# Performance work log

Hardware: AMD Instinct MI355X
Metric: run time of the kernel (lower is better)

Reference implementation:

```python
import jax, jax.numpy as jnp
import numpy as np

FSIZE = 128   # fsize
ANUM = 16     # number of agents
CNUM = 2048   # number of cities
BATCH = 64


def setup_inputs() -> dict:
    key = jax.random.key(0)
    ks = jax.random.split(key, 6)
    f = FSIZE
    N = CNUM + 2 * ANUM
    s = 0.02
    return {
        "nfeature": jax.random.normal(ks[0], (BATCH, f, N), jnp.float32),
        # torch Linear weights are [out, in]
        "Wg": jax.random.normal(ks[1], (f, 4 * f), jnp.float32) * s,   # glb_embedding
        "bg": jnp.zeros((f,), jnp.float32),
        "Wc": jax.random.normal(ks[2], (3 * f, 2 * f), jnp.float32) * s,  # city_embedding
        "bc": jnp.zeros((3 * f,), jnp.float32),
        "Wa": jax.random.normal(ks[3], (f, 3 * f), jnp.float32) * s,   # agent_embedding
        "ba": jnp.zeros((f,), jnp.float32),
        "Wp": jax.random.normal(ks[4], (f, f), jnp.float32) * s,       # project_out
        "bp": jnp.zeros((f,), jnp.float32),
        "step": 1,
        "anum": ANUM,
    }


def reference(nfeature, Wg, bg, Wc, bc, Wa, ba, Wp, bp, step, anum):
    nf = jnp.transpose(nfeature, (0, 2, 1))  # [B, N, f]
    B, N, f = nf.shape
    cnum = N - 2 * anum
    city = nf[:, :cnum]                       # [B, cnum, f]
    a_start = nf[:, cnum:cnum + anum]         # [B, anum, f]
    a_end = nf[:, cnum + anum:]               # [B, anum, f]

    # global context via max pooling over segments -> glb_embedding
    glb = jnp.concatenate([nf.max(1), city.max(1), a_start.max(1), a_end.max(1)], axis=1)  # [B, 4f]
    deglb = (glb @ Wg.T + bg)[:, None, :]     # [B, 1, f]

    # mean-pooled global context -> same glb_embedding -> free agent token
    ave = jnp.concatenate([nf.mean(1), city.mean(1), a_start.mean(1), a_end.mean(1)], axis=1)
    free_agent = (ave @ Wg.T + bg)[:, None, :]  # [B, 1, f]

    # city keys/values/logit-keys: x, y, z
    city_feat = jnp.concatenate([jnp.broadcast_to(deglb, (B, cnum, f)), city], axis=2)  # [B, cnum, 2f]
    xyz = city_feat @ Wc.T + bc               # [B, cnum, 3f]
    x, y, z = jnp.split(xyz, 3, axis=2)       # each [B, cnum, f]

    # agent queries
    agent_feat = jnp.concatenate(
        [jnp.broadcast_to(deglb, (B, anum, f)), a_start, a_end], axis=2)  # [B, anum, 3f]
    af = agent_feat @ Wa.T + ba               # [B, anum, f]
    if step > 0:
        af = jnp.concatenate([af, free_agent], axis=1)  # [B, anum+1, f]

    scale = 1.0 / jnp.sqrt(jnp.float32(f))
    ucj = jnp.einsum('baf,bcf->bac', af, x) * scale           # [B, A, cnum]
    new_af = jnp.einsum('bac,bcf->baf', jax.nn.softmax(ucj, axis=2), y)
    new_af = new_af @ Wp.T + bp                                # project_out
    logits = jnp.tanh(jnp.einsum('baf,bcf->bac', new_af, z) * scale) * 10.0  # [B, A, cnum]
    probs = jax.nn.softmax(jnp.transpose(logits, (0, 2, 1)), axis=2)         # [B, cnum, A]
    return probs
```

## Files before the change

kernel.cpp:

```cpp
#include <hip/hip_runtime.h>
#include <math.h>

#define F 128
#define NTOT 2080
#define CN 2048
#define AN 16
#define NA 17
#define CHK 128
#define NCHK 16

__device__ __forceinline__ float wmax(float v){
  #pragma unroll
  for(int m=32;m;m>>=1) v = fmaxf(v, __shfl_xor(v, m, 64));
  return v;
}
__device__ __forceinline__ float wsum(float v){
  #pragma unroll
  for(int m=32;m;m>>=1) v += __shfl_xor(v, m, 64);
  return v;
}

__global__ __launch_bounds__(256) void k0t_transpose(
      const float* __restrict__ Wg, const float* __restrict__ Wc,
      const float* __restrict__ Wp, const float* __restrict__ Wa,
      float* __restrict__ WgT, float* __restrict__ WcT,
      float* __restrict__ WpT, float* __restrict__ WaT){
  __shared__ float tile[32][33];
  const int z = blockIdx.z;
  const float* src; float* dst; int R, C;
  if(z==0){ src=Wg; dst=WgT; R=128; C=512; }
  else if(z==1){ src=Wc; dst=WcT; R=384; C=256; }
  else if(z==2){ src=Wp; dst=WpT; R=128; C=128; }
  else { src=Wa; dst=WaT; R=128; C=384; }
  const int c0 = blockIdx.x*32, r0 = blockIdx.y*32;
  if(c0>=C || r0>=R) return;
  const int tx = threadIdx.x&31, ty = threadIdx.x>>5;
  #pragma unroll
  for(int rr=0;rr<4;rr++)
    tile[ty+rr*8][tx] = src[(size_t)(r0+ty+rr*8)*C + c0 + tx];
  __syncthreads();
  #pragma unroll
  for(int rr=0;rr<4;rr++)
    dst[(size_t)(c0+ty+rr*8)*R + r0 + tx] = tile[tx][ty+rr*8];
}

__global__ __launch_bounds__(128) void k0a_wpy(const float* __restrict__ Wp, const float* __restrict__ Wc,
                                               float* __restrict__ Wpy){
  const int k = blockIdx.x, i = threadIdx.x;
  float acc = 0.f;
  const float* wp = Wp + (size_t)k*F;
  for(int j=0;j<F;j++) acc += wp[j]*Wc[(size_t)(128+j)*256 + 128 + i];
  Wpy[k*F+i] = acc;
}

__global__ __launch_bounds__(128) void k0b_m1(const float* __restrict__ Wc, const float* __restrict__ Wpy,
                                              float* __restrict__ M1){
  const int jc = blockIdx.x, i = threadIdx.x;
  float acc = 0.f;
  for(int k=0;k<F;k++) acc += Wc[(size_t)(256+k)*256 + 128 + jc]*Wpy[k*F+i];
  M1[jc*F+i] = acc;
}

__global__ __launch_bounds__(256) void k1_reduce(const float* __restrict__ nf,
                                                 float* __restrict__ glb, float* __restrict__ ave){
  const int jg = blockIdx.x, b = blockIdx.y;
  const int w = threadIdx.x>>6, lane = threadIdx.x&63;
  const int j = jg*4 + w;
  const float4* row = (const float4*)(nf + (size_t)(b*F + j)*NTOT);
  float cmax=-INFINITY, csum=0.f, smax=-INFINITY, ssum=0.f, emax=-INFINITY, esum=0.f;
  for(int n4 = lane; n4 < 520; n4 += 64){
    float4 v = row[n4];
    float mx = fmaxf(fmaxf(v.x,v.y), fmaxf(v.z,v.w));
    float sm = (v.x+v.y)+(v.z+v.w);
    if(n4 < 512){ cmax=fmaxf(cmax,mx); csum+=sm; }
    else if(n4 < 516){ smax=fmaxf(smax,mx); ssum+=sm; }
    else { emax=fmaxf(emax,mx); esum+=sm; }
  }
  cmax=wmax(cmax); csum=wsum(csum); smax=wmax(smax); ssum=wsum(ssum); emax=wmax(emax); esum=wsum(esum);
  if(lane==0){
    const int gb = b*4*F;
    glb[gb + j]       = fmaxf(cmax, fmaxf(smax,emax));
    glb[gb + F + j]   = cmax;
    glb[gb + 2*F + j] = smax;
    glb[gb + 3*F + j] = emax;
    float tS = csum+ssum+esum;
    ave[gb + j]       = tS / 2080.f;
    ave[gb + F + j]   = csum / 2048.f;
    ave[gb + 2*F + j] = ssum / 16.f;
    ave[gb + 3*F + j] = esum / 16.f;
  }
}

__global__ __launch_bounds__(256) void k2a_prep(
    const float* __restrict__ WgT, const float* __restrict__ bg,
    const float* __restrict__ WcT, const float* __restrict__ Wc, const float* __restrict__ bc,
    const float* __restrict__ WpT, const float* __restrict__ bp,
    const float* __restrict__ Wpy,
    const float* __restrict__ glb, const float* __restrict__ ave,
    float* __restrict__ deglb_g, float* __restrict__ fa_g, float* __restrict__ cx,
    float* __restrict__ czc, float* __restrict__ vz, float* __restrict__ szc){
  const int b = blockIdx.x, tid = threadIdx.x;
  __shared__ float glb_s[512], ave_s[512];
  __shared__ float deglb_s[F], cvec_s[3*F], cpy_s[F];
  for(int i=tid;i<512;i+=256){ glb_s[i]=glb[b*512+i]; ave_s[i]=ave[b*512+i]; }
  __syncthreads();
  {
    const int j = tid&127;
    const float* src = (tid<128)? glb_s : ave_s;
    float a0=0.f,a1=0.f,a2=0.f,a3=0.f;
    for(int k=0;k<512;k+=4){
      a0 += WgT[(size_t)(k+0)*128+j]*src[k+0];
      a1 += WgT[(size_t)(k+1)*128+j]*src[k+1];
      a2 += WgT[(size_t)(k+2)*128+j]*src[k+2];
      a3 += WgT[(size_t)(k+3)*128+j]*src[k+3];
    }
    float d = (a0+a1)+(a2+a3) + bg[j];
    if(tid<128){ deglb_s[j]=d; deglb_g[b*F+j]=d; }
    else fa_g[b*F+j]=d;
  }
  __syncthreads();
  for(int i=tid;i<3*F;i+=256){
    float a0=0.f,a1=0.f,a2=0.f,a3=0.f;
    for(int k=0;k<F;k+=4){
      a0 += WcT[(size_t)(k+0)*384+i]*deglb_s[k+0];
      a1 += WcT[(size_t)(k+1)*384+i]*deglb_s[k+1];
      a2 += WcT[(size_t)(k+2)*384+i]*deglb_s[k+2];
      a3 += WcT[(size_t)(k+3)*384+i]*deglb_s[k+3];
    }
    float v = (a0+a1)+(a2+a3) + bc[i];
    cvec_s[i]=v;
    if(i<F) cx[b*F+i]=v;
  }
  __syncthreads();
  if(tid<128){
    const int j = tid;
    float a0=0.f,a1=0.f,a2=0.f,a3=0.f;
    for(int k=0;k<F;k+=4){
      a0 += WpT[(size_t)(k+0)*128+j]*cvec_s[128+k+0];
      a1 += WpT[(size_t)(k+1)*128+j]*cvec_s[128+k+1];
      a2 += WpT[(size_t)(k+2)*128+j]*cvec_s[128+k+2];
      a3 += WpT[(size_t)(k+3)*128+j]*cvec_s[128+k+3];
    }
    cpy_s[j] = (a0+a1)+(a2+a3) + bp[j];
  } else {
    const int j = tid-128;
    float a0=0.f,a1=0.f,a2=0.f,a3=0.f;
    for(int k=0;k<F;k+=4){
      a0 += Wpy[(size_t)(k+0)*128+j]*cvec_s[256+k+0];
      a1 += Wpy[(size_t)(k+1)*128+j]*cvec_s[256+k+1];
      a2 += Wpy[(size_t)(k+2)*128+j]*cvec_s[256+k+2];
      a3 += Wpy[(size_t)(k+3)*128+j]*cvec_s[256+k+3];
    }
    vz[b*F+j] = (a0+a1)+(a2+a3);
  }
  __syncthreads();
  if(tid<128){
    const int j = tid;
    float a0=0.f,a1=0.f,a2=0.f,a3=0.f;
    for(int k=0;k<F;k+=4){
      a0 += Wc[(size_t)(256+k+0)*256 + 128 + j]*cpy_s[k+0];
      a1 += Wc[(size_t)(256+k+1)*256 + 128 + j]*cpy_s[k+1];
      a2 += Wc[(size_t)(256+k+2)*256 + 128 + j]*cpy_s[k+2];
      a3 += Wc[(size_t)(256+k+3)*256 + 128 + j]*cpy_s[k+3];
    }
    czc[b*F+j] = (a0+a1)+(a2+a3);
  } else if(tid<192){
    const int lane = tid-128;
    float p = cpy_s[lane]*cvec_s[256+lane] + cpy_s[64+lane]*cvec_s[256+64+lane];
    p = wsum(p);
    if(lane==0) szc[b]=p;
  }
}

__global__ __launch_bounds__(256) void k2c_agents(
    const float* __restrict__ nf, const float* __restrict__ WaT, const float* __restrict__ ba,
    const float* __restrict__ Wc,
    const float* __restrict__ deglb_g, const float* __restrict__ fa_g, const float* __restrict__ cx,
    float* __restrict__ afx, float* __restrict__ sx){
  const int a = blockIdx.x, b = blockIdx.y, tid = threadIdx.x;
  __shared__ float src_s[384];
  __shared__ float af_s[F], cx_s[F];
  if(tid<128){ src_s[tid] = deglb_g[b*F+tid]; cx_s[tid]=cx[b*F+tid]; }
  else if(a<16){
    const int j = tid-128;
    src_s[128+j] = nf[(size_t)(b*F+j)*NTOT + CN + a];
    src_s[256+j] = nf[(size_t)(b*F+j)*NTOT + CN + AN + a];
  }
  __syncthreads();
  if(a<16){
    if(tid<128){
      const int j = tid;
      float a0=0.f,a1=0.f,a2=0.f,a3=0.f;
      for(int k=0;k<384;k+=4){
        a0 += WaT[(size_t)(k+0)*128+j]*src_s[k+0];
        a1 += WaT[(size_t)(k+1)*128+j]*src_s[k+1];
        a2 += WaT[(size_t)(k+2)*128+j]*src_s[k+2];
        a3 += WaT[(size_t)(k+3)*128+j]*src_s[k+3];
      }
      af_s[j] = (a0+a1)+(a2+a3) + ba[j];
    }
  } else if(tid<128){
    af_s[tid] = fa_g[b*F+tid];
  }
  __syncthreads();
  if(tid<128){
    const int j = tid;
    float a0=0.f,a1=0.f,a2=0.f,a3=0.f;
    for(int i=0;i<F;i+=4){
      a0 += af_s[i+0]*Wc[(size_t)(i+0)*256 + 128 + j];
      a1 += af_s[i+1]*Wc[(size_t)(i+1)*256 + 128 + j];
      a2 += af_s[i+2]*Wc[(size_t)(i+2)*256 + 128 + j];
      a3 += af_s[i+3]*Wc[(size_t)(i+3)*256 + 128 + j];
    }
    afx[((size_t)b*NA+a)*F + j] = (a0+a1)+(a2+a3);
  } else if(tid<192){
    const int lane = tid-128;
    float p = af_s[lane]*cx_s[lane] + af_s[64+lane]*cx_s[64+lane];
    p = wsum(p);
    if(lane==0) sx[b*NA+a]=p;
  }
}

__global__ __launch_bounds__(256) void k35_flash(const float* __restrict__ nf,
      const float* __restrict__ afx, const float* __restrict__ sx,
      float* __restrict__ pmax, float* __restrict__ psum, float* __restrict__ tpart){
  const int b = blockIdx.y, tid = threadIdx.x;
  const int chunk = blockIdx.x, c0 = chunk*CHK;
  __shared__ float afx_s[NA*F];
  __shared__ float sx_s[NA];
  __shared__ float at_s[NA*CHK];
  __shared__ float4 nf4_s[F*8];
  __shared__ float red_s[2][NA];
  __shared__ float m_s[NA];
  for(int o=tid;o<NA*F;o+=256) afx_s[o]=afx[(size_t)b*NA*F+o];
  if(tid<NA) sx_s[tid]=sx[b*NA+tid];
  __syncthreads();
  const int h = tid>>7, cl = tid&127, i0 = h*64;
  float acc[NA];
  #pragma unroll
  for(int a=0;a<NA;a++) acc[a]=0.f;
  {
    const float* base = nf + (size_t)b*F*NTOT + (size_t)i0*NTOT + c0 + cl;
    for(int q=0;q<16;q++){
      float v0 = base[(size_t)(q*4+0)*NTOT];
      float v1 = base[(size_t)(q*4+1)*NTOT];
      float v2 = base[(size_t)(q*4+2)*NTOT];
      float v3 = base[(size_t)(q*4+3)*NTOT];
      #pragma unroll
      for(int a=0;a<NA;a++){
        float4 w = *(const float4*)&afx_s[a*F + i0 + q*4];
        acc[a] += w.x*v0 + w.y*v1 + w.z*v2 + w.w*v3;
      }
    }
  }
  if(h==0){
    #pragma unroll
    for(int a=0;a<NA;a++) at_s[a*CHK+cl] = acc[a];
  }
  __syncthreads();
  const int lane = tid&63;
  const float scale = 0.088388347648318447f;
  if(h==1){
    const int wq = (tid>>6)&1;
    #pragma unroll
    for(int a=0;a<NA;a++){
      acc[a] = (acc[a] + at_s[a*CHK+cl] + sx_s[a])*scale;
      float m = wmax(acc[a]);
      if(lane==0) red_s[wq][a]=m;
    }
  }
  __syncthreads();
  if(tid<NA){
    float m = fmaxf(red_s[0][tid], red_s[1][tid]);
    m_s[tid]=m;
    pmax[(b*NA+tid)*NCHK + chunk]=m;
  }
  __syncthreads();
  if(h==1){
    const int wq = (tid>>6)&1;
    #pragma unroll
    for(int a=0;a<NA;a++){
      float e = __expf(acc[a]-m_s[a]);
      at_s[a*CHK+cl]=e;
      float s = wsum(e);
      if(lane==0) red_s[wq][a]=s;
    }
  }
  __syncthreads();
  if(tid<NA)
    psum[(b*NA+tid)*NCHK + chunk] = red_s[0][tid]+red_s[1][tid];
  const int i = tid&127, A0 = h*8;
  float ta[9];
  #pragma unroll
  for(int a=0;a<9;a++) ta[a]=0.f;
  for(int s4=0;s4<4;s4++){
    const int csl = s4*32, cs = c0 + csl;
    __syncthreads();
    for(int idx=tid; idx<F*8; idx+=256){
      const int ii=idx>>3, g=idx&7;
      nf4_s[ii*8 + (g^(ii&7))] = *(const float4*)(nf + (size_t)(b*F+ii)*NTOT + cs + g*4);
    }
    __syncthreads();
    #pragma unroll 2
    for(int g=0; g<8; g++){
      float4 v = nf4_s[i*8 + (g^(i&7))];
      #pragma unroll
      for(int a=0;a<9;a++){
        float4 w = *(const float4*)&at_s[(A0+a)*CHK + csl + g*4];
        ta[a] += w.x*v.x + w.y*v.y + w.z*v.z + w.w*v.w;
      }
    }
  }
  float* dst = tpart + (size_t)chunk*64*NA*F + (size_t)b*NA*F;
  #pragma unroll
  for(int a=0;a<9;a++){
    if(h==0 || a>0) dst[(A0+a)*F + i] = ta[a];
  }
}

__global__ __launch_bounds__(128) void k5c_final(const float* __restrict__ M1,
      const float* __restrict__ tpart, const float* __restrict__ pmax, const float* __restrict__ psum,
      const float* __restrict__ czc, const float* __restrict__ vz, const float* __restrict__ szc,
      float* __restrict__ afz, float* __restrict__ szv){
  const int a = blockIdx.x, b = blockIdx.y, tid = threadIdx.x;
  __shared__ float tn_s[F];
  const float* pm = pmax + (b*NA+a)*NCHK;
  const float* ps = psum + (b*NA+a)*NCHK;
  float M=-INFINITY;
  #pragma unroll
  for(int k=0;k<NCHK;k++) M = fmaxf(M, pm[k]);
  float w[NCHK]; float rs=0.f;
  #pragma unroll
  for(int k=0;k<NCHK;k++){ w[k]=__expf(pm[k]-M); rs += ps[k]*w[k]; }
  float s = 0.f;
  #pragma unroll
  for(int k=0;k<NCHK;k++) s += tpart[(size_t)k*64*NA*F + ((size_t)b*NA+a)*F + tid]*w[k];
  tn_s[tid] = s / rs;
  __syncthreads();
  float acc = 0.f;
  const float* m = M1 + (size_t)tid*F;
  for(int i=0;i<F;i++) acc += m[i]*tn_s[i];
  afz[((size_t)b*NA+a)*F + tid] = acc + czc[b*F+tid];
  float p = tn_s[tid]*vz[b*F+tid];
  p = wsum(p);
  __shared__ float red[2];
  if((tid&63)==0) red[tid>>6]=p;
  __syncthreads();
  if(tid==0) szv[b*NA+a] = red[0]+red[1] + szc[b];
}

__global__ __launch_bounds__(256) void k6_out(const float* __restrict__ nf, const float* __restrict__ afz,
      const float* __restrict__ szv, const int* __restrict__ step, float* __restrict__ out){
  const int b = blockIdx.y, tid = threadIdx.x;
  const int chunk = blockIdx.x, c0 = chunk*CHK;
  __shared__ float afz_s[NA*F]; __shared__ float sz_s[NA];
  __shared__ float sc_s[NA*CHK];
  for(int o=tid;o<NA*F;o+=256) afz_s[o]=afz[(size_t)b*NA*F+o];
  if(tid<NA) sz_s[tid]=szv[b*NA+tid];
  __syncthreads();
  const int h = tid>>7, cl = tid&127, i0 = h*64;
  float acc[NA];
  #pragma unroll
  for(int a=0;a<NA;a++) acc[a]=0.f;
  {
    const float* base = nf + (size_t)b*F*NTOT + (size_t)i0*NTOT + c0 + cl;
    for(int q=0;q<16;q++){
      float v0 = base[(size_t)(q*4+0)*NTOT];
      float v1 = base[(size_t)(q*4+1)*NTOT];
      float v2 = base[(size_t)(q*4+2)*NTOT];
      float v3 = base[(size_t)(q*4+3)*NTOT];
      #pragma unroll
      for(int a=0;a<NA;a++){
        float4 w = *(const float4*)&afz_s[a*F + i0 + q*4];
        acc[a] += w.x*v0 + w.y*v1 + w.z*v2 + w.w*v3;
      }
    }
  }
  if(h==0){
    #pragma unroll
    for(int a=0;a<NA;a++) sc_s[a*CHK+cl] = acc[a];
  }
  __syncthreads();
  if(h==1){
    const int A = (step[0] > 0) ? NA : AN;
    const float scale = 0.088388347648318447f;
    float l[NA];
    #pragma unroll
    for(int a=0;a<NA;a++)
      l[a] = tanhf((acc[a] + sc_s[a*CHK+cl] + sz_s[a])*scale)*10.f;
    const bool f17 = (A==NA);
    float m = l[0];
    #pragma unroll
    for(int a=1;a<AN;a++) m = fmaxf(m,l[a]);
    if(f17) m = fmaxf(m,l[16]);
    float ssum=0.f;
    #pragma unroll
    for(int a=0;a<AN;a++){ float e=__expf(l[a]-m); l[a]=e; ssum+=e; }
    float e16=__expf(l[16]-m);
    if(f17){ ssum+=e16; }
    const float inv = 1.f/ssum;
    float* op = out + (size_t)(b*CN + c0 + cl)*A;
    #pragma unroll
    for(int a=0;a<AN;a++) op[a]=l[a]*inv;
    if(f17) op[16]=e16*inv;
  }
}

extern "C" void kernel_launch(void* const* d_in, const int* in_sizes, int n_in,
                              void* d_out, int out_size, void* d_ws, size_t ws_size,
                              hipStream_t stream){
  const float* nf = (const float*)d_in[0];
  const float* Wg = (const float*)d_in[1];
  const float* bg = (const float*)d_in[2];
  const float* Wc = (const float*)d_in[3];
  const float* bc = (const float*)d_in[4];
  const float* Wa = (const float*)d_in[5];
  const float* ba = (const float*)d_in[6];
  const float* Wp = (const float*)d_in[7];
  const float* bp = (const float*)d_in[8];
  const int*  step = (const int*)d_in[9];
  float* out = (float*)d_out;

  float* ws = (float*)d_ws;
  float* glb     = ws;
  float* ave     = glb + 64*512;
  float* afx     = ave + 64*512;
  float* sx      = afx + 64*NA*F;
  float* Wpy     = sx + 64*NA;
  float* M1      = Wpy + F*F;
  float* czc     = M1 + F*F;
  float* vz      = czc + 64*F;
  float* szc     = vz + 64*F;
  float* pmax    = szc + 64;
  float* psum    = pmax + 64*NA*NCHK;
  float* deglb_g = psum + 64*NA*NCHK;
  float* fa_g    = deglb_g + 64*F;
  float* cx      = fa_g + 64*F;
  float* WgT     = cx + 64*F;
  float* WcT     = WgT + 512*F;
  float* WpT     = WcT + 256*384;
  float* WaT     = WpT + F*F;
  float* tpart   = WaT + 384*F;
  float* afz     = tpart + (size_t)NCHK*64*NA*F;
  float* szv     = afz + 64*NA*F;

  k0t_transpose<<<dim3(16,12,4),256,0,stream>>>(Wg,Wc,Wp,Wa, WgT,WcT,WpT,WaT);
  k0a_wpy<<<F,F,0,stream>>>(Wp, Wc, Wpy);
  k0b_m1<<<F,F,0,stream>>>(Wc, Wpy, M1);
  k1_reduce<<<dim3(32,64),256,0,stream>>>(nf, glb, ave);
  k2a_prep<<<64,256,0,stream>>>(WgT,bg, WcT,Wc,bc, WpT,bp, Wpy, glb,ave, deglb_g,fa_g,cx, czc,vz,szc);
  k2c_agents<<<dim3(NA,64),256,0,stream>>>(nf, WaT,ba,Wc, deglb_g,fa_g,cx, afx,sx);
  k35_flash<<<dim3(NCHK,64),256,0,stream>>>(nf, afx, sx, pmax, psum, tpart);
  k5c_final<<<dim3(NA,64),128,0,stream>>>(M1, tpart, pmax, psum, czc, vz, szc, afz, szv);
  k6_out<<<dim3(NCHK,64),256,0,stream>>>(nf, afz, szv, step, out);
}
```

Measured before the change: 153.0 us.

## Re-tile flash and output kernels with float2 loads and 4-way K split

Both score GEMV phases now give each thread two adjacent cities with float2 loads and split the 128-wide feature reduction across four wavefronts instead of two. The partial sums are combined through shared memory in a serialized four-step accumulation. The softmax statistics are spread over all 256 threads, each half handling about nine agents, instead of leaving half the block idle. The P·V phase has each thread compute two feature rows over half the groups, with a shared-memory reduction before the store. This aims for better register reuse of the shared weights and wider global loads, at the cost of extra barriers and a reduction pass.

Measured after the change: 162.4 us. 1.06x slower.

```diff
diff --git a/kernel.cpp b/kernel.cpp
--- a/kernel.cpp
+++ b/kernel.cpp
@@ -230,69 +230,83 @@
   __shared__ float sx_s[NA];
   __shared__ float at_s[NA*CHK];
   __shared__ float4 nf4_s[F*8];
-  __shared__ float red_s[2][NA];
-  __shared__ float m_s[NA];
+  __shared__ float red_s[4][NA], red2_s[4][NA];
   for(int o=tid;o<NA*F;o+=256) afx_s[o]=afx[(size_t)b*NA*F+o];
   if(tid<NA) sx_s[tid]=sx[b*NA+tid];
   __syncthreads();
-  const int h = tid>>7, cl = tid&127, i0 = h*64;
-  float acc[NA];
-  #pragma unroll
-  for(int a=0;a<NA;a++) acc[a]=0.f;
+  const int kq = tid>>6;
+  const int ct = tid&63;
+  const int lane = tid&63, w = tid>>6;
+  float2 acc[NA];
+  #pragma unroll
+  for(int a=0;a<NA;a++){ acc[a].x=0.f; acc[a].y=0.f; }
   {
-    const float* base = nf + (size_t)b*F*NTOT + (size_t)i0*NTOT + c0 + cl;
-    for(int q=0;q<16;q++){
-      float v0 = base[(size_t)(q*4+0)*NTOT];
-      float v1 = base[(size_t)(q*4+1)*NTOT];
-      float v2 = base[(size_t)(q*4+2)*NTOT];
-      float v3 = base[(size_t)(q*4+3)*NTOT];
+    const float* base = nf + (size_t)b*F*NTOT + (size_t)(kq*32)*NTOT + c0 + 2*ct;
+    #pragma unroll 2
+    for(int q=0;q<8;q++){
+      float2 l0 = *(const float2*)(base + (size_t)(q*4+0)*NTOT);
+      float2 l1 = *(const float2*)(base + (size_t)(q*4+1)*NTOT);
+      float2 l2 = *(const float2*)(base + (size_t)(q*4+2)*NTOT);
+      float2 l3 = *(const float2*)(base + (size_t)(q*4+3)*NTOT);
       #pragma unroll
       for(int a=0;a<NA;a++){
-        float4 w = *(const float4*)&afx_s[a*F + i0 + q*4];
-        acc[a] += w.x*v0 + w.y*v1 + w.z*v2 + w.w*v3;
-      }
-    }
-  }
-  if(h==0){
-    #pragma unroll
-    for(int a=0;a<NA;a++) at_s[a*CHK+cl] = acc[a];
-  }
-  __syncthreads();
-  const int lane = tid&63;
+        float4 wv = *(const float4*)&afx_s[a*F + kq*32 + q*4];
+        acc[a].x += wv.x*l0.x + wv.y*l1.x + wv.z*l2.x + wv.w*l3.x;
+        acc[a].y += wv.x*l0.y + wv.y*l1.y + wv.z*l2.y + wv.w*l3.y;
+      }
+    }
+  }
+  for(int k=0;k<4;k++){
+    __syncthreads();
+    if(kq==k){
+      #pragma unroll
+      for(int a=0;a<NA;a++){
+        float2* p = (float2*)&at_s[a*CHK + 2*ct];
+        if(k==0){ *p = acc[a]; }
+        else { float2 v = *p; v.x += acc[a].x; v.y += acc[a].y; *p = v; }
+      }
+    }
+  }
+  __syncthreads();
+  const int cl = tid&127;
+  const int hh = tid>>7;
+  const int aBeg = hh? 9:0;
   const float scale = 0.088388347648318447f;
-  if(h==1){
-    const int wq = (tid>>6)&1;
-    #pragma unroll
-    for(int a=0;a<NA;a++){
-      acc[a] = (acc[a] + at_s[a*CHK+cl] + sx_s[a])*scale;
-      float m = wmax(acc[a]);
-      if(lane==0) red_s[wq][a]=m;
+  float sc[9];
+  #pragma unroll
+  for(int a2=0;a2<9;a2++){
+    const int a = aBeg+a2;
+    if(a<NA){
+      sc[a2] = (at_s[a*CHK+cl] + sx_s[a])*scale;
+      float mx = wmax(sc[a2]);
+      if(lane==0) red_s[w][a]=mx;
+    }
+  }
+  __syncthreads();
+  #pragma unroll
+  for(int a2=0;a2<9;a2++){
+    const int a = aBeg+a2;
+    if(a<NA){
+      float m = fmaxf(red_s[hh*2][a], red_s[hh*2+1][a]);
+      float e = __expf(sc[a2]-m);
+      at_s[a*CHK+cl] = e;
+      float s = wsum(e);
+      if(lane==0) red2_s[w][a]=s;
     }
   }
   __syncthreads();
   if(tid<NA){
-    float m = fmaxf(red_s[0][tid], red_s[1][tid]);
-    m_s[tid]=m;
-    pmax[(b*NA+tid)*NCHK + chunk]=m;
-  }
-  __syncthreads();
-  if(h==1){
-    const int wq = (tid>>6)&1;
-    #pragma unroll
-    for(int a=0;a<NA;a++){
-      float e = __expf(acc[a]-m_s[a]);
-      at_s[a*CHK+cl]=e;
-      float s = wsum(e);
-      if(lane==0) red_s[wq][a]=s;
-    }
-  }
-  __syncthreads();
-  if(tid<NA)
-    psum[(b*NA+tid)*NCHK + chunk] = red_s[0][tid]+red_s[1][tid];
-  const int i = tid&127, A0 = h*8;
-  float ta[9];
-  #pragma unroll
-  for(int a=0;a<9;a++) ta[a]=0.f;
+    const int base = (tid<9)? 0 : 2;
+    pmax[(b*NA+tid)*NCHK + chunk] = fmaxf(red_s[base][tid], red_s[base+1][tid]);
+    psum[(b*NA+tid)*NCHK + chunk] = red2_s[base][tid] + red2_s[base+1][tid];
+  }
+  const int i1 = tid&63;
+  const int g2 = (tid>>6)&1;
+  const int h  = tid>>7;
+  const int A0 = h*8;
+  float ta0[9], ta1[9];
+  #pragma unroll
+  for(int a=0;a<9;a++){ ta0[a]=0.f; ta1[a]=0.f; }
   for(int s4=0;s4<4;s4++){
     const int csl = s4*32, cs = c0 + csl;
     __syncthreads();
@@ -301,20 +315,38 @@
       nf4_s[ii*8 + (g^(ii&7))] = *(const float4*)(nf + (size_t)(b*F+ii)*NTOT + cs + g*4);
     }
     __syncthreads();
-    #pragma unroll 2
-    for(int g=0; g<8; g++){
-      float4 v = nf4_s[i*8 + (g^(i&7))];
+    #pragma unroll
+    for(int gg=0; gg<4; gg++){
+      const int g = gg*2 + g2;
+      float4 v0 = nf4_s[i1*8 + (g^(i1&7))];
+      float4 v1 = nf4_s[(i1+64)*8 + (g^(i1&7))];
       #pragma unroll
       for(int a=0;a<9;a++){
-        float4 w = *(const float4*)&at_s[(A0+a)*CHK + csl + g*4];
-        ta[a] += w.x*v.x + w.y*v.y + w.z*v.z + w.w*v.w;
-      }
-    }
-  }
-  float* dst = tpart + (size_t)chunk*64*NA*F + (size_t)b*NA*F;
-  #pragma unroll
-  for(int a=0;a<9;a++){
-    if(h==0 || a>0) dst[(A0+a)*F + i] = ta[a];
+        float4 wv = *(const float4*)&at_s[(A0+a)*CHK + csl + g*4];
+        ta0[a] += wv.x*v0.x + wv.y*v0.y + wv.z*v0.z + wv.w*v0.w;
+        ta1[a] += wv.x*v1.x + wv.y*v1.y + wv.z*v1.z + wv.w*v1.w;
+      }
+    }
+  }
+  float* pt = afx_s;
+  __syncthreads();
+  if(g2==1){
+    #pragma unroll
+    for(int a=0;a<9;a++){
+      pt[(A0+a)*F + i1]      = ta0[a];
+      pt[(A0+a)*F + i1 + 64] = ta1[a];
+    }
+  }
+  __syncthreads();
+  if(g2==0){
+    float* dst = tpart + (size_t)chunk*64*NA*F + (size_t)b*NA*F;
+    #pragma unroll
+    for(int a=0;a<9;a++){
+      if(h==0 || a>0){
+        dst[(A0+a)*F + i1]      = ta0[a] + pt[(A0+a)*F + i1];
+        dst[(A0+a)*F + i1 + 64] = ta1[a] + pt[(A0+a)*F + i1 + 64];
+      }
+    }
   }
 }
 
@@ -358,36 +390,46 @@
   for(int o=tid;o<NA*F;o+=256) afz_s[o]=afz[(size_t)b*NA*F+o];
   if(tid<NA) sz_s[tid]=szv[b*NA+tid];
   __syncthreads();
-  const int h = tid>>7, cl = tid&127, i0 = h*64;
-  float acc[NA];
-  #pragma unroll
-  for(int a=0;a<NA;a++) acc[a]=0.f;
+  const int kq = tid>>6, ct = tid&63;
+  float2 acc[NA];
+  #pragma unroll
+  for(int a=0;a<NA;a++){ acc[a].x=0.f; acc[a].y=0.f; }
   {
-    const float* base = nf + (size_t)b*F*NTOT + (size_t)i0*NTOT + c0 + cl;
-    for(int q=0;q<16;q++){
-      float v0 = base[(size_t)(q*4+0)*NTOT];
-      float v1 = base[(size_t)(q*4+1)*NTOT];
-      float v2 = base[(size_t)(q*4+2)*NTOT];
-      float v3 = base[(size_t)(q*4+3)*NTOT];
+    const float* base = nf + (size_t)b*F*NTOT + (size_t)(kq*32)*NTOT + c0 + 2*ct;
+    #pragma unroll 2
+    for(int q=0;q<8;q++){
+      float2 l0 = *(const float2*)(base + (size_t)(q*4+0)*NTOT);
+      float2 l1 = *(const float2*)(base + (size_t)(q*4+1)*NTOT);
+      float2 l2 = *(const float2*)(base + (size_t)(q*4+2)*NTOT);
+      float2 l3 = *(const float2*)(base + (size_t)(q*4+3)*NTOT);
       #pragma unroll
       for(int a=0;a<NA;a++){
-        float4 w = *(const float4*)&afz_s[a*F + i0 + q*4];
-        acc[a] += w.x*v0 + w.y*v1 + w.z*v2 + w.w*v3;
-      }
-    }
-  }
-  if(h==0){
-    #pragma unroll
-    for(int a=0;a<NA;a++) sc_s[a*CHK+cl] = acc[a];
-  }
-  __syncthreads();
-  if(h==1){
+        float4 wv = *(const float4*)&afz_s[a*F + kq*32 + q*4];
+        acc[a].x += wv.x*l0.x + wv.y*l1.x + wv.z*l2.x + wv.w*l3.x;
+        acc[a].y += wv.x*l0.y + wv.y*l1.y + wv.z*l2.y + wv.w*l3.y;
+      }
+    }
+  }
+  for(int k=0;k<4;k++){
+    __syncthreads();
+    if(kq==k){
+      #pragma unroll
+      for(int a=0;a<NA;a++){
+        float2* p = (float2*)&sc_s[a*CHK + 2*ct];
+        if(k==0){ *p = acc[a]; }
+        else { float2 v = *p; v.x += acc[a].x; v.y += acc[a].y; *p = v; }
+      }
+    }
+  }
+  __syncthreads();
+  if(tid<128){
+    const int cl = tid;
     const int A = (step[0] > 0) ? NA : AN;
     const float scale = 0.088388347648318447f;
     float l[NA];
     #pragma unroll
     for(int a=0;a<NA;a++)
-      l[a] = tanhf((acc[a] + sc_s[a*CHK+cl] + sz_s[a])*scale)*10.f;
+      l[a] = tanhf((sc_s[a*CHK+cl] + sz_s[a])*scale)*10.f;
     const bool f17 = (A==NA);
     float m = l[0];
     #pragma unroll
```

## Double city chunk per block and compute two columns per thread

Applied to the files above, without the earlier changes.

Raises the city chunk from 128 to 256, so each block covers twice as many cities and each thread accumulates two city columns, reusing every shared-memory weight float4 for two nf values. The softmax-statistics and output-softmax phases now run on all 256 threads, one city each, instead of only the upper half, which removes idle threads in those phases. The cost is half as many blocks (8 chunks × 64 batches), which lowers parallelism on the GPU, along with doubled accumulator registers and larger shared memory per block, both of which could reduce occupancy.

Result: slower. 156.7 us (+2.4%).

```diff
diff --git a/kernel.cpp b/kernel.cpp
--- a/kernel.cpp
+++ b/kernel.cpp
@@ -6,8 +6,8 @@
 #define CN 2048
 #define AN 16
 #define NA 17
-#define CHK 128
-#define NCHK 16
+#define CHK 256
+#define NCHK 8
 
 __device__ __forceinline__ float wmax(float v){
   #pragma unroll
@@ -230,71 +230,77 @@
   __shared__ float sx_s[NA];
   __shared__ float at_s[NA*CHK];
   __shared__ float4 nf4_s[F*8];
-  __shared__ float red_s[2][NA];
-  __shared__ float m_s[NA];
+  __shared__ float red_s[4][NA], red2_s[4][NA], m_s[NA];
   for(int o=tid;o<NA*F;o+=256) afx_s[o]=afx[(size_t)b*NA*F+o];
   if(tid<NA) sx_s[tid]=sx[b*NA+tid];
   __syncthreads();
   const int h = tid>>7, cl = tid&127, i0 = h*64;
-  float acc[NA];
-  #pragma unroll
-  for(int a=0;a<NA;a++) acc[a]=0.f;
+  float a0v[NA], a1v[NA];
+  #pragma unroll
+  for(int a=0;a<NA;a++){ a0v[a]=0.f; a1v[a]=0.f; }
   {
     const float* base = nf + (size_t)b*F*NTOT + (size_t)i0*NTOT + c0 + cl;
+    #pragma unroll 2
     for(int q=0;q<16;q++){
-      float v0 = base[(size_t)(q*4+0)*NTOT];
-      float v1 = base[(size_t)(q*4+1)*NTOT];
-      float v2 = base[(size_t)(q*4+2)*NTOT];
-      float v3 = base[(size_t)(q*4+3)*NTOT];
+      const float* r = base + (size_t)(q*4)*NTOT;
+      float v0 = r[0],      u0 = r[128];
+      float v1 = r[NTOT],   u1 = r[NTOT+128];
+      float v2 = r[2*NTOT], u2 = r[2*NTOT+128];
+      float v3 = r[3*NTOT], u3 = r[3*NTOT+128];
       #pragma unroll
       for(int a=0;a<NA;a++){
-        float4 w = *(const float4*)&afx_s[a*F + i0 + q*4];
-        acc[a] += w.x*v0 + w.y*v1 + w.z*v2 + w.w*v3;
+        float4 wv = *(const float4*)&afx_s[a*F + i0 + q*4];
+        a0v[a] += wv.x*v0 + wv.y*v1 + wv.z*v2 + wv.w*v3;
+        a1v[a] += wv.x*u0 + wv.y*u1 + wv.z*u2 + wv.w*u3;
       }
     }
   }
   if(h==0){
     #pragma unroll
-    for(int a=0;a<NA;a++) at_s[a*CHK+cl] = acc[a];
-  }
-  __syncthreads();
-  const int lane = tid&63;
+    for(int a=0;a<NA;a++){ at_s[a*CHK+cl]=a0v[a]; at_s[a*CHK+cl+128]=a1v[a]; }
+  }
+  __syncthreads();
   const float scale = 0.088388347648318447f;
   if(h==1){
-    const int wq = (tid>>6)&1;
     #pragma unroll
     for(int a=0;a<NA;a++){
-      acc[a] = (acc[a] + at_s[a*CHK+cl] + sx_s[a])*scale;
-      float m = wmax(acc[a]);
-      if(lane==0) red_s[wq][a]=m;
-    }
+      at_s[a*CHK+cl]     = (at_s[a*CHK+cl]     + a0v[a] + sx_s[a])*scale;
+      at_s[a*CHK+cl+128] = (at_s[a*CHK+cl+128] + a1v[a] + sx_s[a])*scale;
+    }
+  }
+  __syncthreads();
+  const int lane = tid&63, w = tid>>6;
+  float sc[NA];
+  #pragma unroll
+  for(int a=0;a<NA;a++){
+    sc[a] = at_s[a*CHK+tid];
+    float mx = wmax(sc[a]);
+    if(lane==0) red_s[w][a]=mx;
   }
   __syncthreads();
   if(tid<NA){
-    float m = fmaxf(red_s[0][tid], red_s[1][tid]);
+    float m = fmaxf(fmaxf(red_s[0][tid],red_s[1][tid]), fmaxf(red_s[2][tid],red_s[3][tid]));
     m_s[tid]=m;
     pmax[(b*NA+tid)*NCHK + chunk]=m;
   }
   __syncthreads();
-  if(h==1){
-    const int wq = (tid>>6)&1;
-    #pragma unroll
-    for(int a=0;a<NA;a++){
-      float e = __expf(acc[a]-m_s[a]);
-      at_s[a*CHK+cl]=e;
-      float s = wsum(e);
-      if(lane==0) red_s[wq][a]=s;
-    }
+  #pragma unroll
+  for(int a=0;a<NA;a++){
+    float e = __expf(sc[a]-m_s[a]);
+    at_s[a*CHK+tid]=e;
+    float s = wsum(e);
+    if(lane==0) red2_s[w][a]=s;
   }
   __syncthreads();
   if(tid<NA)
-    psum[(b*NA+tid)*NCHK + chunk] = red_s[0][tid]+red_s[1][tid];
-  const int i = tid&127, A0 = h*8;
+    psum[(b*NA+tid)*NCHK + chunk] =
+      (red2_s[0][tid]+red2_s[1][tid])+(red2_s[2][tid]+red2_s[3][tid]);
+  const int i = tid&127, A0 = (tid>>7)*8;
   float ta[9];
   #pragma unroll
   for(int a=0;a<9;a++) ta[a]=0.f;
-  for(int s4=0;s4<4;s4++){
-    const int csl = s4*32, cs = c0 + csl;
+  for(int s8=0;s8<8;s8++){
+    const int csl = s8*32, cs = c0 + csl;
     __syncthreads();
     for(int idx=tid; idx<F*8; idx+=256){
       const int ii=idx>>3, g=idx&7;
@@ -306,15 +312,15 @@
       float4 v = nf4_s[i*8 + (g^(i&7))];
       #pragma unroll
       for(int a=0;a<9;a++){
-        float4 w = *(const float4*)&at_s[(A0+a)*CHK + csl + g*4];
-        ta[a] += w.x*v.x + w.y*v.y + w.z*v.z + w.w*v.w;
+        float4 wv = *(const float4*)&at_s[(A0+a)*CHK + csl + g*4];
+        ta[a] += wv.x*v.x + wv.y*v.y + wv.z*v.z + wv.w*v.w;
       }
     }
   }
   float* dst = tpart + (size_t)chunk*64*NA*F + (size_t)b*NA*F;
   #pragma unroll
   for(int a=0;a<9;a++){
-    if(h==0 || a>0) dst[(A0+a)*F + i] = ta[a];
+    if(tid<128 || a>0) dst[(A0+a)*F + i] = ta[a];
   }
 }
 
@@ -353,41 +359,54 @@
       const float* __restrict__ szv, const int* __restrict__ step, float* __restrict__ out){
   const int b = blockIdx.y, tid = threadIdx.x;
   const int chunk = blockIdx.x, c0 = chunk*CHK;
-  __shared__ float afz_s[NA*F]; __shared__ float sz_s[NA];
-  __shared__ float sc_s[NA*CHK];
+  __shared__ float afz_s[NA*F];
+  __shared__ float sz_s[NA];
+  __shared__ float at_s[NA*CHK];
   for(int o=tid;o<NA*F;o+=256) afz_s[o]=afz[(size_t)b*NA*F+o];
   if(tid<NA) sz_s[tid]=szv[b*NA+tid];
   __syncthreads();
   const int h = tid>>7, cl = tid&127, i0 = h*64;
-  float acc[NA];
-  #pragma unroll
-  for(int a=0;a<NA;a++) acc[a]=0.f;
+  float a0v[NA], a1v[NA];
+  #pragma unroll
+  for(int a=0;a<NA;a++){ a0v[a]=0.f; a1v[a]=0.f; }
   {
     const float* base = nf + (size_t)b*F*NTOT + (size_t)i0*NTOT + c0 + cl;
+    #pragma unroll 2
     for(int q=0;q<16;q++){
-      float v0 = base[(size_t)(q*4+0)*NTOT];
-      float v1 = base[(size_t)(q*4+1)*NTOT];
-      float v2 = base[(size_t)(q*4+2)*NTOT];
-      float v3 = base[(size_t)(q*4+3)*NTOT];
+      const float* r = base + (size_t)(q*4)*NTOT;
+      float v0 = r[0],      u0 = r[128];
+      float v1 = r[NTOT],   u1 = r[NTOT+128];
+      float v2 = r[2*NTOT], u2 = r[2*NTOT+128];
+      float v3 = r[3*NTOT], u3 = r[3*NTOT+128];
       #pragma unroll
       for(int a=0;a<NA;a++){
-        float4 w = *(const float4*)&afz_s[a*F + i0 + q*4];
-        acc[a] += w.x*v0 + w.y*v1 + w.z*v2 + w.w*v3;
+        float4 wv = *(const float4*)&afz_s[a*F + i0 + q*4];
+        a0v[a] += wv.x*v0 + wv.y*v1 + wv.z*v2 + wv.w*v3;
+        a1v[a] += wv.x*u0 + wv.y*u1 + wv.z*u2 + wv.w*u3;
       }
     }
   }
   if(h==0){
     #pragma unroll
-    for(int a=0;a<NA;a++) sc_s[a*CHK+cl] = acc[a];
+    for(int a=0;a<NA;a++){ at_s[a*CHK+cl]=a0v[a]; at_s[a*CHK+cl+128]=a1v[a]; }
   }
   __syncthreads();
   if(h==1){
+    #pragma unroll
+    for(int a=0;a<NA;a++){
+      at_s[a*CHK+cl]     += a0v[a];
+      at_s[a*CHK+cl+128] += a1v[a];
+    }
+  }
+  __syncthreads();
+  {
+    const int c = tid;
     const int A = (step[0] > 0) ? NA : AN;
     const float scale = 0.088388347648318447f;
     float l[NA];
     #pragma unroll
     for(int a=0;a<NA;a++)
-      l[a] = tanhf((acc[a] + sc_s[a*CHK+cl] + sz_s[a])*scale)*10.f;
+      l[a] = tanhf((at_s[a*CHK+c] + sz_s[a])*scale)*10.f;
     const bool f17 = (A==NA);
     float m = l[0];
     #pragma unroll
@@ -399,7 +418,7 @@
     float e16=__expf(l[16]-m);
     if(f17){ ssum+=e16; }
     const float inv = 1.f/ssum;
-    float* op = out + (size_t)(b*CN + c0 + cl)*A;
+    float* op = out + (size_t)(b*CN + c0 + c)*A;
     #pragma unroll
     for(int a=0;a<AN;a++) op[a]=l[a]*inv;
     if(f17) op[16]=e16*inv;
```

## Merge preprocessing kernels into two launches and use direct global-to-LDS loads

Applied to the files above, without the earlier changes.

Merges the weight transposes, Wpy product and feature reductions into one launch, and folds the M1 product into the prep kernel as extra blocks, cutting five launches down to two. In the flash kernel the nf tile staging now uses global_load_lds to write straight into shared memory instead of going through registers, keeping the XOR swizzle by permuting the source address. The aim is to remove launch gaps and register round-trips. The risk is that independent work now sits in one grid and can load-balance unevenly, and the direct LDS load path depends on hardware support.

New measurement: 136.5 us. 1.12x faster.

```diff
diff --git a/kernel.cpp b/kernel.cpp
--- a/kernel.cpp
+++ b/kernel.cpp
@@ -1,5 +1,6 @@
 #include <hip/hip_runtime.h>
 #include <math.h>
+#include <stdint.h>
 
 #define F 128
 #define NTOT 2080
@@ -20,86 +21,94 @@
   return v;
 }
 
-__global__ __launch_bounds__(256) void k0t_transpose(
+__global__ __launch_bounds__(256) void k_pre1(
+      const float* __restrict__ nf,
       const float* __restrict__ Wg, const float* __restrict__ Wc,
       const float* __restrict__ Wp, const float* __restrict__ Wa,
       float* __restrict__ WgT, float* __restrict__ WcT,
-      float* __restrict__ WpT, float* __restrict__ WaT){
+      float* __restrict__ WpT, float* __restrict__ WaT,
+      float* __restrict__ Wpy,
+      float* __restrict__ glb, float* __restrict__ ave){
   __shared__ float tile[32][33];
-  const int z = blockIdx.z;
-  const float* src; float* dst; int R, C;
-  if(z==0){ src=Wg; dst=WgT; R=128; C=512; }
-  else if(z==1){ src=Wc; dst=WcT; R=384; C=256; }
-  else if(z==2){ src=Wp; dst=WpT; R=128; C=128; }
-  else { src=Wa; dst=WaT; R=128; C=384; }
-  const int c0 = blockIdx.x*32, r0 = blockIdx.y*32;
-  if(c0>=C || r0>=R) return;
-  const int tx = threadIdx.x&31, ty = threadIdx.x>>5;
-  #pragma unroll
-  for(int rr=0;rr<4;rr++)
-    tile[ty+rr*8][tx] = src[(size_t)(r0+ty+rr*8)*C + c0 + tx];
-  __syncthreads();
-  #pragma unroll
-  for(int rr=0;rr<4;rr++)
-    dst[(size_t)(c0+ty+rr*8)*R + r0 + tx] = tile[tx][ty+rr*8];
-}
-
-__global__ __launch_bounds__(128) void k0a_wpy(const float* __restrict__ Wp, const float* __restrict__ Wc,
-                                               float* __restrict__ Wpy){
-  const int k = blockIdx.x, i = threadIdx.x;
-  float acc = 0.f;
-  const float* wp = Wp + (size_t)k*F;
-  for(int j=0;j<F;j++) acc += wp[j]*Wc[(size_t)(128+j)*256 + 128 + i];
-  Wpy[k*F+i] = acc;
-}
-
-__global__ __launch_bounds__(128) void k0b_m1(const float* __restrict__ Wc, const float* __restrict__ Wpy,
-                                              float* __restrict__ M1){
-  const int jc = blockIdx.x, i = threadIdx.x;
-  float acc = 0.f;
-  for(int k=0;k<F;k++) acc += Wc[(size_t)(256+k)*256 + 128 + jc]*Wpy[k*F+i];
-  M1[jc*F+i] = acc;
-}
-
-__global__ __launch_bounds__(256) void k1_reduce(const float* __restrict__ nf,
-                                                 float* __restrict__ glb, float* __restrict__ ave){
-  const int jg = blockIdx.x, b = blockIdx.y;
-  const int w = threadIdx.x>>6, lane = threadIdx.x&63;
-  const int j = jg*4 + w;
-  const float4* row = (const float4*)(nf + (size_t)(b*F + j)*NTOT);
-  float cmax=-INFINITY, csum=0.f, smax=-INFINITY, ssum=0.f, emax=-INFINITY, esum=0.f;
-  for(int n4 = lane; n4 < 520; n4 += 64){
-    float4 v = row[n4];
-    float mx = fmaxf(fmaxf(v.x,v.y), fmaxf(v.z,v.w));
-    float sm = (v.x+v.y)+(v.z+v.w);
-    if(n4 < 512){ cmax=fmaxf(cmax,mx); csum+=sm; }
-    else if(n4 < 516){ smax=fmaxf(smax,mx); ssum+=sm; }
-    else { emax=fmaxf(emax,mx); esum+=sm; }
-  }
-  cmax=wmax(cmax); csum=wsum(csum); smax=wmax(smax); ssum=wsum(ssum); emax=wmax(emax); esum=wsum(esum);
-  if(lane==0){
-    const int gb = b*4*F;
-    glb[gb + j]       = fmaxf(cmax, fmaxf(smax,emax));
-    glb[gb + F + j]   = cmax;
-    glb[gb + 2*F + j] = smax;
-    glb[gb + 3*F + j] = emax;
-    float tS = csum+ssum+esum;
-    ave[gb + j]       = tS / 2080.f;
-    ave[gb + F + j]   = csum / 2048.f;
-    ave[gb + 2*F + j] = ssum / 16.f;
-    ave[gb + 3*F + j] = esum / 16.f;
-  }
-}
-
-__global__ __launch_bounds__(256) void k2a_prep(
+  const int bx = blockIdx.x, tid = threadIdx.x;
+  if(bx < 768){
+    const int z = bx/192, rem = bx%192;
+    const int c0 = (rem&15)*32, r0 = (rem>>4)*32;
+    const float* src; float* dst; int R, C;
+    if(z==0){ src=Wg; dst=WgT; R=128; C=512; }
+    else if(z==1){ src=Wc; dst=WcT; R=384; C=256; }
+    else if(z==2){ src=Wp; dst=WpT; R=128; C=128; }
+    else { src=Wa; dst=WaT; R=128; C=384; }
+    if(c0>=C || r0>=R) return;
+    const int tx = tid&31, ty = tid>>5;
+    #pragma unroll
+    for(int rr=0;rr<4;rr++)
+      tile[ty+rr*8][tx] = src[(size_t)(r0+ty+rr*8)*C + c0 + tx];
+    __syncthreads();
+    #pragma unroll
+    for(int rr=0;rr<4;rr++)
+      dst[(size_t)(c0+ty+rr*8)*R + r0 + tx] = tile[tx][ty+rr*8];
+    return;
+  }
+  if(bx < 832){
+    const int k = (bx-768)*2 + (tid>>7);
+    const int i = tid&127;
+    float acc = 0.f;
+    const float* wp = Wp + (size_t)k*F;
+    for(int j=0;j<F;j++) acc += wp[j]*Wc[(size_t)(128+j)*256 + 128 + i];
+    Wpy[k*F+i] = acc;
+    return;
+  }
+  {
+    const int r = bx-832;
+    const int jg = r&31, b = r>>5;
+    const int w = tid>>6, lane = tid&63;
+    const int j = jg*4 + w;
+    const float4* row = (const float4*)(nf + (size_t)(b*F + j)*NTOT);
+    float cmax=-INFINITY, csum=0.f, smax=-INFINITY, ssum=0.f, emax=-INFINITY, esum=0.f;
+    for(int n4 = lane; n4 < 520; n4 += 64){
+      float4 v = row[n4];
+      float mx = fmaxf(fmaxf(v.x,v.y), fmaxf(v.z,v.w));
+      float sm = (v.x+v.y)+(v.z+v.w);
+      if(n4 < 512){ cmax=fmaxf(cmax,mx); csum+=sm; }
+      else if(n4 < 516){ smax=fmaxf(smax,mx); ssum+=sm; }
+      else { emax=fmaxf(emax,mx); esum+=sm; }
+    }
+    cmax=wmax(cmax); csum=wsum(csum); smax=wmax(smax); ssum=wsum(ssum); emax=wmax(emax); esum=wsum(esum);
+    if(lane==0){
+      const int gb = b*4*F;
+      glb[gb + j]       = fmaxf(cmax, fmaxf(smax,emax));
+      glb[gb + F + j]   = cmax;
+      glb[gb + 2*F + j] = smax;
+      glb[gb + 3*F + j] = emax;
+      float tS = csum+ssum+esum;
+      ave[gb + j]       = tS / 2080.f;
+      ave[gb + F + j]   = csum / 2048.f;
+      ave[gb + 2*F + j] = ssum / 16.f;
+      ave[gb + 3*F + j] = esum / 16.f;
+    }
+  }
+}
+
+__global__ __launch_bounds__(256) void k_pre2(
     const float* __restrict__ WgT, const float* __restrict__ bg,
     const float* __restrict__ WcT, const float* __restrict__ Wc, const float* __restrict__ bc,
     const float* __restrict__ WpT, const float* __restrict__ bp,
     const float* __restrict__ Wpy,
     const float* __restrict__ glb, const float* __restrict__ ave,
     float* __restrict__ deglb_g, float* __restrict__ fa_g, float* __restrict__ cx,
-    float* __restrict__ czc, float* __restrict__ vz, float* __restrict__ szc){
-  const int b = blockIdx.x, tid = threadIdx.x;
+    float* __restrict__ czc, float* __restrict__ vz, float* __restrict__ szc,
+    float* __restrict__ M1){
+  const int bx = blockIdx.x, tid = threadIdx.x;
+  if(bx >= 64){
+    const int jc = (bx-64)*2 + (tid>>7);
+    const int i = tid&127;
+    float acc = 0.f;
+    for(int k=0;k<F;k++) acc += Wc[(size_t)(256+k)*256 + 128 + jc]*Wpy[(size_t)k*F+i];
+    M1[jc*F+i] = acc;
+    return;
+  }
+  const int b = bx;
   __shared__ float glb_s[512], ave_s[512];
   __shared__ float deglb_s[F], cvec_s[3*F], cpy_s[F];
   for(int i=tid;i<512;i+=256){ glb_s[i]=glb[b*512+i]; ave_s[i]=ave[b*512+i]; }
@@ -297,8 +306,10 @@
     const int csl = s4*32, cs = c0 + csl;
     __syncthreads();
     for(int idx=tid; idx<F*8; idx+=256){
-      const int ii=idx>>3, g=idx&7;
-      nf4_s[ii*8 + (g^(ii&7))] = *(const float4*)(nf + (size_t)(b*F+ii)*NTOT + cs + g*4);
+      const int ii=idx>>3, gp=idx&7, g=gp^(ii&7);
+      __builtin_amdgcn_global_load_lds(
+        (const __attribute__((address_space(1))) void*)(nf + (size_t)(b*F+ii)*NTOT + cs + g*4),
+        (__attribute__((address_space(3))) void*)&nf4_s[idx], 16, 0, 0);
     }
     __syncthreads();
     #pragma unroll 2
@@ -444,11 +455,9 @@
   float* afz     = tpart + (size_t)NCHK*64*NA*F;
   float* szv     = afz + 64*NA*F;
 
-  k0t_transpose<<<dim3(16,12,4),256,0,stream>>>(Wg,Wc,Wp,Wa, WgT,WcT,WpT,WaT);
-  k0a_wpy<<<F,F,0,stream>>>(Wp, Wc, Wpy);
-  k0b_m1<<<F,F,0,stream>>>(Wc, Wpy, M1);
-  k1_reduce<<<dim3(32,64),256,0,stream>>>(nf, glb, ave);
-  k2a_prep<<<64,256,0,stream>>>(WgT,bg, WcT,Wc,bc, WpT,bp, Wpy, glb,ave, deglb_g,fa_g,cx, czc,vz,szc);
+  k_pre1<<<2880,256,0,stream>>>(nf, Wg,Wc,Wp,Wa, WgT,WcT,WpT,WaT, Wpy, glb,ave);
+  k_pre2<<<128,256,0,stream>>>(WgT,bg, WcT,Wc,bc, WpT,bp, Wpy, glb,ave,
+                               deglb_g,fa_g,cx, czc,vz,szc, M1);
   k2c_agents<<<dim3(NA,64),256,0,stream>>>(nf, WaT,ba,Wc, deglb_g,fa_g,cx, afx,sx);
   k35_flash<<<dim3(NCHK,64),256,0,stream>>>(nf, afx, sx, pmax, psum, tpart);
   k5c_final<<<dim3(NA,64),128,0,stream>>>(M1, tpart, pmax, psum, czc, vz, szc, afz, szv);
```
